# Optimization experiments

Measured on AMD Instinct MI355X. Metric: run time of the kernel, lower is better.

## Reference

```python
import jax, jax.numpy as jnp
import numpy as np

K = 4  # Chebyshev order (init kwarg k)


def _spmm(rows, cols, vals, x, n_nodes):
    # sparse [N,N] @ dense [N,D] via gather + segment_sum
    return jax.ops.segment_sum(vals[:, None] * x[cols], rows, num_segments=n_nodes)


def setup_inputs() -> dict:
    key = jax.random.key(0)
    k_x, k_r, k_c, k_v, k_w = jax.random.split(key, 5)
    N, E, D_IN, D_OUT = 50000, 800000, 128, 128
    inp = {
        "input": jax.random.normal(k_x, (N, D_IN), dtype=jnp.float32),
        "adj_rows": jax.random.randint(k_r, (E,), 0, N, dtype=jnp.int32),
        "adj_cols": jax.random.randint(k_c, (E,), 0, N, dtype=jnp.int32),
        "adj_vals": jax.random.uniform(k_v, (E,), dtype=jnp.float32) * 0.1,
        # xavier_uniform for W [in_dim, out_dim]
        "W": jax.random.uniform(k_w, (D_IN, D_OUT), dtype=jnp.float32,
                                 minval=-1.0, maxval=1.0) * np.sqrt(6.0 / (D_IN + D_OUT)),
    }
    return inp


def reference(input, adj_rows, adj_cols, adj_vals, W):
    n = input.shape[0]
    xs = []
    for i in range(K):
        if i == 0:
            xs.append(input @ W)
        elif i == 1:
            # faithful to original: support computed but unused; xs[1] == xs[0]
            xs.append(input @ W)
        else:
            support = _spmm(adj_rows, adj_cols, 2.0 * adj_vals, xs[i - 1], n) - xs[i - 2]
            xs.append(support @ W)
    return xs[-1]
```

## Files before the change

### kernel.cpp

```cpp
#include <hip/hip_runtime.h>
#include <cstddef>
#include <cstdint>

#define THREADS 256
#define KPART 256
#define MAXNB 1600

typedef short bf16x8 __attribute__((ext_vector_type(8)));
typedef float f32x4 __attribute__((ext_vector_type(4)));
typedef unsigned short u16x8 __attribute__((ext_vector_type(8)));

#define GLOBAL_AS __attribute__((address_space(1)))
#define LDS_AS    __attribute__((address_space(3)))

__device__ __forceinline__ void async_copy16(const void* g, void* l) {
    __builtin_amdgcn_global_load_lds((const GLOBAL_AS void*)g, (LDS_AS void*)l, 16, 0, 0);
}

__device__ __forceinline__ ushort f2bf(float f) {
    uint32_t u = __float_as_uint(f);
    u = u + 0x7FFFu + ((u >> 16) & 1u);
    return (ushort)(u >> 16);
}
__device__ __forceinline__ float bf2f(ushort h) {
    return __uint_as_float(((uint32_t)h) << 16);
}

__device__ __forceinline__ void rowfma(float4& acc, const float4 xv,
                                       const float4 w0, const float4 w1,
                                       const float4 w2, const float4 w3) {
    acc.x = fmaf(xv.x, w0.x, acc.x); acc.y = fmaf(xv.x, w0.y, acc.y);
    acc.z = fmaf(xv.x, w0.z, acc.z); acc.w = fmaf(xv.x, w0.w, acc.w);
    acc.x = fmaf(xv.y, w1.x, acc.x); acc.y = fmaf(xv.y, w1.y, acc.y);
    acc.z = fmaf(xv.y, w1.z, acc.z); acc.w = fmaf(xv.y, w1.w, acc.w);
    acc.x = fmaf(xv.z, w2.x, acc.x); acc.y = fmaf(xv.z, w2.y, acc.y);
    acc.z = fmaf(xv.z, w2.z, acc.z); acc.w = fmaf(xv.z, w2.w, acc.w);
    acc.x = fmaf(xv.w, w3.x, acc.x); acc.y = fmaf(xv.w, w3.y, acc.y);
    acc.z = fmaf(xv.w, w3.z, acc.z); acc.w = fmaf(xv.w, w3.w, acc.w);
}

__device__ __forceinline__ void mm32(const float4* Ws4, const float4* Xs4,
                                     int c4, int rb,
                                     float4& a0, float4& a1, float4& a2, float4& a3) {
#pragma unroll 4
    for (int kq = 0; kq < 32; ++kq) {
        float4 w0 = Ws4[(4 * kq + 0) * 32 + c4];
        float4 w1 = Ws4[(4 * kq + 1) * 32 + c4];
        float4 w2 = Ws4[(4 * kq + 2) * 32 + c4];
        float4 w3 = Ws4[(4 * kq + 3) * 32 + c4];
        float4 x0 = Xs4[(rb + 0) * 32 + kq];
        float4 x1 = Xs4[(rb + 1) * 32 + kq];
        float4 x2 = Xs4[(rb + 2) * 32 + kq];
        float4 x3 = Xs4[(rb + 3) * 32 + kq];
        rowfma(a0, x0, w0, w1, w2, w3);
        rowfma(a1, x1, w0, w1, w2, w3);
        rowfma(a2, x2, w0, w1, w2, w3);
        rowfma(a3, x3, w0, w1, w2, w3);
    }
}

__global__ __launch_bounds__(256, 2)
void wpow_kernel(const float* __restrict__ W,
                 ushort* __restrict__ w3t_hi, ushort* __restrict__ w3t_lo,
                 ushort* __restrict__ nw2t_hi, ushort* __restrict__ nw2t_lo) {
    __shared__ float4 Ws4[128 * 32];
    __shared__ float4 Xs4[32 * 32];
    const int tid = threadIdx.x;
    const int row0 = (blockIdx.x & 3) * 32;
    const bool is3 = blockIdx.x >= 4;
    const float4* __restrict__ W4 = (const float4*)W;

#pragma unroll
    for (int i = 0; i < 16; ++i) Ws4[tid + i * 256] = W4[tid + i * 256];
#pragma unroll
    for (int i = 0; i < 4; ++i) {
        int li = tid + i * 256;
        Xs4[li] = W4[(size_t)(row0 + (li >> 5)) * 32 + (li & 31)];
    }
    __syncthreads();

    const int c4 = tid & 31;
    const int rb = (tid >> 5) * 4;
    float4 a0 = {0.f, 0.f, 0.f, 0.f};
    float4 a1 = {0.f, 0.f, 0.f, 0.f};
    float4 a2 = {0.f, 0.f, 0.f, 0.f};
    float4 a3 = {0.f, 0.f, 0.f, 0.f};
    mm32(Ws4, Xs4, c4, rb, a0, a1, a2, a3);

    if (is3) {
        __syncthreads();
        Xs4[(rb + 0) * 32 + c4] = a0;
        Xs4[(rb + 1) * 32 + c4] = a1;
        Xs4[(rb + 2) * 32 + c4] = a2;
        Xs4[(rb + 3) * 32 + c4] = a3;
        __syncthreads();
        a0 = {0.f, 0.f, 0.f, 0.f};
        a1 = {0.f, 0.f, 0.f, 0.f};
        a2 = {0.f, 0.f, 0.f, 0.f};
        a3 = {0.f, 0.f, 0.f, 0.f};
        mm32(Ws4, Xs4, c4, rb, a0, a1, a2, a3);
    }

    ushort* __restrict__ dh = is3 ? w3t_hi : nw2t_hi;
    ushort* __restrict__ dl = is3 ? w3t_lo : nw2t_lo;
    const float sgn = is3 ? 1.0f : -1.0f;
    const int r = row0 + rb;
#pragma unroll
    for (int i = 0; i < 4; ++i) {
        float4 a = (i == 0) ? a0 : (i == 1) ? a1 : (i == 2) ? a2 : a3;
        const int k = r + i;
#pragma unroll
        for (int e = 0; e < 4; ++e) {
            float v = ((e == 0) ? a.x : (e == 1) ? a.y : (e == 2) ? a.z : a.w) * sgn;
            int c = c4 * 4 + e;
            int idx = c * 128 + (k ^ ((c & 7) << 3));
            ushort h = f2bf(v);
            dh[idx] = h;
            dl[idx] = f2bf(v - bf2f(h));
        }
    }
}

__global__ __launch_bounds__(256, 2)
void gemm_dual_mfma(const float* __restrict__ A1, const ushort* __restrict__ B1h,
                    const ushort* __restrict__ B1l,
                    const float* __restrict__ A2, const ushort* __restrict__ B2h,
                    const ushort* __restrict__ B2l,
                    float* __restrict__ out, int N) {
    __shared__ ushort WtHi[16384];
    __shared__ ushort WtLo[16384];
    __shared__ ushort XsHi[4096];
    __shared__ ushort XsLo[4096];
    const int tid = threadIdx.x;
    const int row0 = blockIdx.x * 32;
    const int l = tid & 63, w = tid >> 6;
    const int mt = w & 1, ntb = (w >> 1) * 4;
    const int fr = l & 15, fh = l >> 4;

    f32x4 acc[4];
#pragma unroll
    for (int nt = 0; nt < 4; ++nt) acc[nt] = (f32x4){0.f, 0.f, 0.f, 0.f};

    for (int pass = 0; pass < 2; ++pass) {
        const float* __restrict__ Asrc = pass ? A2 : A1;
        const ushort* __restrict__ Bh = pass ? B2h : B1h;
        const ushort* __restrict__ Bl = pass ? B2l : B1l;
        if (pass) __syncthreads();

#pragma unroll
        for (int i = 0; i < 8; ++i) {
            async_copy16(Bh + tid * 8 + i * 2048, WtHi + tid * 8 + i * 2048);
            async_copy16(Bl + tid * 8 + i * 2048, WtLo + tid * 8 + i * 2048);
        }

        {
            const int row = tid >> 3, kb = (tid & 7) * 16;
            int gr = row0 + row;
            if (gr >= N) gr = N - 1;
            const float4* __restrict__ ap =
                (const float4*)(Asrc + (size_t)gr * 128) + (kb >> 2);
            float4 v0 = ap[0], v1 = ap[1], v2 = ap[2], v3 = ap[3];
            float f[16] = {v0.x, v0.y, v0.z, v0.w, v1.x, v1.y, v1.z, v1.w,
                           v2.x, v2.y, v2.z, v2.w, v3.x, v3.y, v3.z, v3.w};
            ushort hi[16], lo[16];
#pragma unroll
            for (int i = 0; i < 16; ++i) {
                hi[i] = f2bf(f[i]);
                lo[i] = f2bf(f[i] - bf2f(hi[i]));
            }
#pragma unroll
            for (int g = 0; g < 2; ++g) {
                int idx = row * 128 + ((kb + 8 * g) ^ ((row & 7) << 3));
                bf16x8 vh, vl;
#pragma unroll
                for (int j = 0; j < 8; ++j) {
                    vh[j] = (short)hi[8 * g + j];
                    vl[j] = (short)lo[8 * g + j];
                }
                *(bf16x8*)&XsHi[idx] = vh;
                *(bf16x8*)&XsLo[idx] = vl;
            }
        }
        __syncthreads();

#pragma unroll
        for (int ks = 0; ks < 4; ++ks) {
            const int arow = mt * 16 + fr;
            const int aoff = arow * 128 + ((ks * 32 + fh * 8) ^ ((arow & 7) << 3));
            bf16x8 ah = *(const bf16x8*)&XsHi[aoff];
            bf16x8 al = *(const bf16x8*)&XsLo[aoff];
#pragma unroll
            for (int nt = 0; nt < 4; ++nt) {
                const int brow = (ntb + nt) * 16 + fr;
                const int boff = brow * 128 + ((ks * 32 + fh * 8) ^ ((brow & 7) << 3));
                bf16x8 bh = *(const bf16x8*)&WtHi[boff];
                bf16x8 bl = *(const bf16x8*)&WtLo[boff];
                acc[nt] = __builtin_amdgcn_mfma_f32_16x16x32_bf16(ah, bh, acc[nt], 0, 0, 0);
                acc[nt] = __builtin_amdgcn_mfma_f32_16x16x32_bf16(al, bh, acc[nt], 0, 0, 0);
                acc[nt] = __builtin_amdgcn_mfma_f32_16x16x32_bf16(ah, bl, acc[nt], 0, 0, 0);
            }
        }
    }

#pragma unroll
    for (int nt = 0; nt < 4; ++nt) {
        const int col = (ntb + nt) * 16 + fr;
#pragma unroll
        for (int i = 0; i < 4; ++i) {
            const int rr = row0 + mt * 16 + fh * 4 + i;
            if (rr < N) out[(size_t)rr * 128 + col] = acc[nt][i];
        }
    }
}

__global__ void part_count_conv_kernel(const int* __restrict__ erows, int E,
                                       int* __restrict__ blockcounts, int NB, int chunk,
                                       const float* __restrict__ X,
                                       ushort* __restrict__ Xbf, int ngroups, int cb) {
    __shared__ int hist[MAXNB];
    const int b = blockIdx.x;
    const int tid = threadIdx.x;
    if (b < cb) {
        int i = b * 256 + tid;
        if (i < ngroups) {
            const float4* __restrict__ X4 = (const float4*)X;
            float4 v0 = X4[i * 2 + 0];
            float4 v1 = X4[i * 2 + 1];
            u16x8 o;
            o[0] = f2bf(v0.x); o[1] = f2bf(v0.y); o[2] = f2bf(v0.z); o[3] = f2bf(v0.w);
            o[4] = f2bf(v1.x); o[5] = f2bf(v1.y); o[6] = f2bf(v1.z); o[7] = f2bf(v1.w);
            ((u16x8*)Xbf)[i] = o;
        }
        return;
    }
    const int k = b - cb;
    for (int i = tid; i < NB; i += 256) hist[i] = 0;
    __syncthreads();
    const int e0 = k * chunk;
    const int e1 = (e0 + chunk < E) ? e0 + chunk : E;
    for (int i = e0 + tid; i < e1; i += 256)
        atomicAdd(&hist[erows[i] >> 5], 1);
    __syncthreads();
    for (int i = tid; i < NB; i += 256) blockcounts[i * KPART + k] = hist[i];
}

__global__ void part_scan1_kernel(int* __restrict__ blockcounts,
                                  int* __restrict__ btotal, int NB) {
    const int tid = threadIdx.x;
    const int lane = tid & 63;
    const int b = blockIdx.x * 4 + (tid >> 6);
    if (b >= NB) return;
    int* __restrict__ row = blockcounts + (size_t)b * KPART;
    int c0 = row[lane * 4 + 0];
    int c1 = row[lane * 4 + 1];
    int c2 = row[lane * 4 + 2];
    int c3 = row[lane * 4 + 3];
    int lsum = c0 + c1 + c2 + c3;
    int s = lsum;
#pragma unroll
    for (int off = 1; off < 64; off <<= 1) {
        int t = __shfl_up(s, off);
        if (lane >= off) s += t;
    }
    int run = s - lsum;
    row[lane * 4 + 0] = run; run += c0;
    row[lane * 4 + 1] = run; run += c1;
    row[lane * 4 + 2] = run; run += c2;
    row[lane * 4 + 3] = run;
    if (lane == 63) btotal[b] = s;
}

__global__ __launch_bounds__(1024)
void part_scan2_kernel(const int* __restrict__ btotal, int* __restrict__ bbase,
                       int NB, int E, int* __restrict__ rowptr, int N) {
    __shared__ int sums[1024];
    const int tid = threadIdx.x;
    const int items = (NB + 1023) >> 10;
    const int start = tid * items;
    const int end = (start + items < NB) ? start + items : NB;
    int s = 0;
    for (int i = start; i < end; ++i) s += btotal[i];
    sums[tid] = s;
    __syncthreads();
#pragma unroll
    for (int off = 1; off < 1024; off <<= 1) {
        int t = (tid >= off) ? sums[tid - off] : 0;
        __syncthreads();
        sums[tid] += t;
        __syncthreads();
    }
    int run = sums[tid] - s;
    for (int i = start; i < end; ++i) {
        bbase[i] = run;
        run += btotal[i];
    }
    if (tid == 0) { bbase[NB] = E; rowptr[N] = E; }
}

__global__ void part_place_kernel(const int* __restrict__ erows,
                                  const int* __restrict__ ecols,
                                  const float* __restrict__ evals, int E,
                                  const int* __restrict__ blockcounts,
                                  const int* __restrict__ bbase, int NB, int chunk,
                                  int2* __restrict__ bucketed) {
    __shared__ int cur[MAXNB];
    const int k = blockIdx.x;
    const int tid = threadIdx.x;
    for (int i = tid; i < NB; i += 256)
        cur[i] = bbase[i] + blockcounts[(size_t)i * KPART + k];
    __syncthreads();
    const int e0 = k * chunk;
    const int e1 = (e0 + chunk < E) ? e0 + chunk : E;
    for (int i = e0 + tid; i < e1; i += 256) {
        int r = erows[i];
        int pos = atomicAdd(&cur[r >> 5], 1);
        int2 p;
        p.x = (int)(((uint32_t)(r & 31) << 16) | (uint32_t)ecols[i]);
        p.y = __float_as_int(2.0f * evals[i]);
        bucketed[pos] = p;
    }
}

__global__ void part_finish_kernel(const int2* __restrict__ bucketed,
                                   const int* __restrict__ bbase,
                                   int* __restrict__ rowptr,
                                   int2* __restrict__ csr, int N) {
    __shared__ int rcnt[32];
    __shared__ int rpos[32];
    const int b = blockIdx.x;
    const int tid = threadIdx.x;
    const int base = bbase[b];
    const int end = bbase[b + 1];
    const int row0 = b * 32;
    if (tid < 32) rcnt[tid] = 0;
    __syncthreads();
    for (int i = base + tid; i < end; i += 256)
        atomicAdd(&rcnt[((uint32_t)bucketed[i].x) >> 16], 1);
    __syncthreads();
    if (tid == 0) {
        int run = base;
        for (int j = 0; j < 32; ++j) {
            int c = rcnt[j];
            rpos[j] = run;
            if (row0 + j < N) rowptr[row0 + j] = run;
            run += c;
        }
    }
    __syncthreads();
    for (int i = base + tid; i < end; i += 256) {
        int2 e = bucketed[i];
        uint32_t meta = (uint32_t)e.x;
        int pos = atomicAdd(&rpos[meta >> 16], 1);
        int2 p;
        p.x = (int)(meta & 0xFFFFu);
        p.y = e.y;
        csr[pos] = p;
    }
}

__device__ __forceinline__ void bf8_fma(float4& aLo, float4& aHi, uint4 v, float s) {
    aLo.x = fmaf(s, __uint_as_float(v.x << 16), aLo.x);
    aLo.y = fmaf(s, __uint_as_float(v.x & 0xFFFF0000u), aLo.y);
    aLo.z = fmaf(s, __uint_as_float(v.y << 16), aLo.z);
    aLo.w = fmaf(s, __uint_as_float(v.y & 0xFFFF0000u), aLo.w);
    aHi.x = fmaf(s, __uint_as_float(v.z << 16), aHi.x);
    aHi.y = fmaf(s, __uint_as_float(v.z & 0xFFFF0000u), aHi.y);
    aHi.z = fmaf(s, __uint_as_float(v.w << 16), aHi.z);
    aHi.w = fmaf(s, __uint_as_float(v.w & 0xFFFF0000u), aHi.w);
}

template <bool WRITE_BF>
__global__ __launch_bounds__(256, 6)
void spmm_gather_bf(const int* __restrict__ rowptr, const int2* __restrict__ csr,
                    const ushort* __restrict__ src, const float* __restrict__ init,
                    void* __restrict__ dst, int N) {
    long long idx = (long long)blockIdx.x * blockDim.x + threadIdx.x;
    int row = (int)(idx >> 4);
    if (row >= N) return;
    int lane = (int)(idx & 15);
    const uint4* __restrict__ S = (const uint4*)src;
    float4 aLo0 = {0.f, 0.f, 0.f, 0.f}, aHi0 = {0.f, 0.f, 0.f, 0.f};
    float4 aLo1 = {0.f, 0.f, 0.f, 0.f}, aHi1 = {0.f, 0.f, 0.f, 0.f};
    if (init) {
        const float4* __restrict__ ip = (const float4*)init + (size_t)row * 32 + lane * 2;
        float4 t0 = ip[0], t1 = ip[1];
        aLo0.x = -t0.x; aLo0.y = -t0.y; aLo0.z = -t0.z; aLo0.w = -t0.w;
        aHi0.x = -t1.x; aHi0.y = -t1.y; aHi0.z = -t1.z; aHi0.w = -t1.w;
    }
    int p = rowptr[row];
    const int p1 = rowptr[row + 1];
    for (; p + 7 < p1; p += 8) {
        int2 cv0 = csr[p + 0];
        int2 cv1 = csr[p + 1];
        int2 cv2 = csr[p + 2];
        int2 cv3 = csr[p + 3];
        int2 cv4 = csr[p + 4];
        int2 cv5 = csr[p + 5];
        int2 cv6 = csr[p + 6];
        int2 cv7 = csr[p + 7];
        uint4 x0 = S[(size_t)cv0.x * 16 + lane];
        uint4 x1 = S[(size_t)cv1.x * 16 + lane];
        uint4 x2 = S[(size_t)cv2.x * 16 + lane];
        uint4 x3 = S[(size_t)cv3.x * 16 + lane];
        uint4 x4 = S[(size_t)cv4.x * 16 + lane];
        uint4 x5 = S[(size_t)cv5.x * 16 + lane];
        uint4 x6 = S[(size_t)cv6.x * 16 + lane];
        uint4 x7 = S[(size_t)cv7.x * 16 + lane];
        bf8_fma(aLo0, aHi0, x0, __int_as_float(cv0.y));
        bf8_fma(aLo1, aHi1, x1, __int_as_float(cv1.y));
        bf8_fma(aLo0, aHi0, x2, __int_as_float(cv2.y));
        bf8_fma(aLo1, aHi1, x3, __int_as_float(cv3.y));
        bf8_fma(aLo0, aHi0, x4, __int_as_float(cv4.y));
        bf8_fma(aLo1, aHi1, x5, __int_as_float(cv5.y));
        bf8_fma(aLo0, aHi0, x6, __int_as_float(cv6.y));
        bf8_fma(aLo1, aHi1, x7, __int_as_float(cv7.y));
    }
    for (; p + 3 < p1; p += 4) {
        int2 cv0 = csr[p + 0];
        int2 cv1 = csr[p + 1];
        int2 cv2 = csr[p + 2];
        int2 cv3 = csr[p + 3];
        uint4 x0 = S[(size_t)cv0.x * 16 + lane];
        uint4 x1 = S[(size_t)cv1.x * 16 + lane];
        uint4 x2 = S[(size_t)cv2.x * 16 + lane];
        uint4 x3 = S[(size_t)cv3.x * 16 + lane];
        bf8_fma(aLo0, aHi0, x0, __int_as_float(cv0.y));
        bf8_fma(aLo1, aHi1, x1, __int_as_float(cv1.y));
        bf8_fma(aLo0, aHi0, x2, __int_as_float(cv2.y));
        bf8_fma(aLo1, aHi1, x3, __int_as_float(cv3.y));
    }
    for (; p < p1; ++p) {
        int2 cv = csr[p];
        uint4 x = S[(size_t)cv.x * 16 + lane];
        bf8_fma(aLo0, aHi0, x, __int_as_float(cv.y));
    }
    float4 lo, hi;
    lo.x = aLo0.x + aLo1.x; lo.y = aLo0.y + aLo1.y;
    lo.z = aLo0.z + aLo1.z; lo.w = aLo0.w + aLo1.w;
    hi.x = aHi0.x + aHi1.x; hi.y = aHi0.y + aHi1.y;
    hi.z = aHi0.z + aHi1.z; hi.w = aHi0.w + aHi1.w;
    if (WRITE_BF) {
        u16x8 o;
        o[0] = f2bf(lo.x); o[1] = f2bf(lo.y); o[2] = f2bf(lo.z); o[3] = f2bf(lo.w);
        o[4] = f2bf(hi.x); o[5] = f2bf(hi.y); o[6] = f2bf(hi.z); o[7] = f2bf(hi.w);
        ((u16x8*)dst)[(size_t)row * 16 + lane] = o;
    } else {
        float4* __restrict__ op = (float4*)dst + (size_t)row * 32 + lane * 2;
        op[0] = lo;
        op[1] = hi;
    }
}

extern "C" void kernel_launch(void* const* d_in, const int* in_sizes, int n_in,
                              void* d_out, int out_size, void* d_ws, size_t ws_size,
                              hipStream_t stream) {
    const float* X     = (const float*)d_in[0];
    const int*   erows = (const int*)d_in[1];
    const int*   ecols = (const int*)d_in[2];
    const float* evals = (const float*)d_in[3];
    const float* W     = (const float*)d_in[4];
    float* out = (float*)d_out;

    const int N = in_sizes[0] / 128;
    const int E = in_sizes[1];

    ushort* t2bf    = (ushort*)d_ws;
    float*  u2      = (float*)(t2bf + (size_t)N * 128);
    int2*   bucketed= (int2*)u2;
    ushort* xbf     = (ushort*)(u2 + (size_t)N * 128);
    ushort* wtab    = xbf + (size_t)N * 128;
    ushort* w3t_hi  = wtab;
    ushort* w3t_lo  = wtab + 16384;
    ushort* nw2t_hi = wtab + 32768;
    ushort* nw2t_lo = wtab + 49152;
    int2*   csr     = (int2*)(wtab + 65536);
    int*    rowptr  = (int*)(csr + E);
    int*    blkcnt  = rowptr + (N + 1);
    const int NB    = (N + 31) >> 5;
    int*    btotal  = blkcnt + (size_t)NB * KPART;
    int*    bbase   = btotal + NB;

    const int chunk    = (E + KPART - 1) / KPART;
    const int ngroups  = N * 16;
    const int cb       = (ngroups + 255) / 256;
    const int g_blocks = (int)(((long long)N * 16 + 255) / 256);
    const int d_blocks = (N + 31) / 32;

    wpow_kernel<<<8, THREADS, 0, stream>>>(W, w3t_hi, w3t_lo, nw2t_hi, nw2t_lo);

    part_count_conv_kernel<<<cb + KPART, THREADS, 0, stream>>>(erows, E, blkcnt, NB,
                                                               chunk, X, xbf, ngroups, cb);
    part_scan1_kernel<<<(NB + 3) / 4, THREADS, 0, stream>>>(blkcnt, btotal, NB);
    part_scan2_kernel<<<1, 1024, 0, stream>>>(btotal, bbase, NB, E, rowptr, N);
    part_place_kernel<<<KPART, THREADS, 0, stream>>>(erows, ecols, evals, E, blkcnt,
                                                     bbase, NB, chunk, bucketed);
    part_finish_kernel<<<NB, THREADS, 0, stream>>>(bucketed, bbase, rowptr, csr, N);

    spmm_gather_bf<true><<<g_blocks, THREADS, 0, stream>>>(rowptr, csr, xbf, X, t2bf, N);
    spmm_gather_bf<false><<<g_blocks, THREADS, 0, stream>>>(rowptr, csr, t2bf, nullptr, u2, N);
    gemm_dual_mfma<<<d_blocks, THREADS, 0, stream>>>(u2, w3t_hi, w3t_lo,
                                                     X, nw2t_hi, nw2t_lo, out, N);
}
```

Measured before the change: 179.8 us.

## Pack CSR entries to 32 bits and slice SpMM gather across feature quarters

CSR entries now pack a 16-bit column index and a bf16 edge value into one 32-bit word, halving index traffic. The SpMM kernels are restructured so each block handles 32 rows for one quarter of the feature dimension, with 8 lanes per row gathering 8-byte chunks. It adds nontemporal loads for CSR and a nontemporal store for the fp32 output, and takes the subtracted initial term from the bf16 copy of X instead of fp32 X. This trades numerical precision (bf16 edge weights and init) and smaller per-lane gathers for less index bandwidth and possibly better cache locality. It also assumes column indices fit in 16 bits.

```diff
diff --git a/kernel.cpp b/kernel.cpp
--- a/kernel.cpp
+++ b/kernel.cpp
@@ -324,7 +324,7 @@
 __global__ void part_finish_kernel(const int2* __restrict__ bucketed,
                                    const int* __restrict__ bbase,
                                    int* __restrict__ rowptr,
-                                   int2* __restrict__ csr, int N) {
+                                   uint32_t* __restrict__ csr, int N) {
     __shared__ int rcnt[32];
     __shared__ int rpos[32];
     const int b = blockIdx.x;
@@ -351,103 +351,95 @@
         int2 e = bucketed[i];
         uint32_t meta = (uint32_t)e.x;
         int pos = atomicAdd(&rpos[meta >> 16], 1);
-        int2 p;
-        p.x = (int)(meta & 0xFFFFu);
-        p.y = e.y;
-        csr[pos] = p;
-    }
-}
-
-__device__ __forceinline__ void bf8_fma(float4& aLo, float4& aHi, uint4 v, float s) {
-    aLo.x = fmaf(s, __uint_as_float(v.x << 16), aLo.x);
-    aLo.y = fmaf(s, __uint_as_float(v.x & 0xFFFF0000u), aLo.y);
-    aLo.z = fmaf(s, __uint_as_float(v.y << 16), aLo.z);
-    aLo.w = fmaf(s, __uint_as_float(v.y & 0xFFFF0000u), aLo.w);
-    aHi.x = fmaf(s, __uint_as_float(v.z << 16), aHi.x);
-    aHi.y = fmaf(s, __uint_as_float(v.z & 0xFFFF0000u), aHi.y);
-    aHi.z = fmaf(s, __uint_as_float(v.w << 16), aHi.z);
-    aHi.w = fmaf(s, __uint_as_float(v.w & 0xFFFF0000u), aHi.w);
-}
-
-template <bool WRITE_BF>
-__global__ __launch_bounds__(256, 6)
-void spmm_gather_bf(const int* __restrict__ rowptr, const int2* __restrict__ csr,
-                    const ushort* __restrict__ src, const float* __restrict__ init,
-                    void* __restrict__ dst, int N) {
-    long long idx = (long long)blockIdx.x * blockDim.x + threadIdx.x;
-    int row = (int)(idx >> 4);
+        csr[pos] = ((meta & 0xFFFFu) << 16) | (uint32_t)f2bf(__int_as_float(e.y));
+    }
+}
+
+__device__ __forceinline__ void fma4bf(float4& a, float v, ushort4 x) {
+    a.x = fmaf(v, bf2f(x.x), a.x);
+    a.y = fmaf(v, bf2f(x.y), a.y);
+    a.z = fmaf(v, bf2f(x.z), a.z);
+    a.w = fmaf(v, bf2f(x.w), a.w);
+}
+
+template <bool WRITE_BF, bool INIT_SUB>
+__global__ __launch_bounds__(256, 8)
+void spmm_slice(const int* __restrict__ rowptr, const uint32_t* __restrict__ csr,
+                const ushort* __restrict__ src, void* __restrict__ dst, int N) {
+    const int s = blockIdx.x & 3;
+    const int g = blockIdx.x >> 2;
+    const int fl = threadIdx.x & 7;
+    const int row = g * 32 + (threadIdx.x >> 3);
     if (row >= N) return;
-    int lane = (int)(idx & 15);
-    const uint4* __restrict__ S = (const uint4*)src;
-    float4 aLo0 = {0.f, 0.f, 0.f, 0.f}, aHi0 = {0.f, 0.f, 0.f, 0.f};
-    float4 aLo1 = {0.f, 0.f, 0.f, 0.f}, aHi1 = {0.f, 0.f, 0.f, 0.f};
-    if (init) {
-        const float4* __restrict__ ip = (const float4*)init + (size_t)row * 32 + lane * 2;
-        float4 t0 = ip[0], t1 = ip[1];
-        aLo0.x = -t0.x; aLo0.y = -t0.y; aLo0.z = -t0.z; aLo0.w = -t0.w;
-        aHi0.x = -t1.x; aHi0.y = -t1.y; aHi0.z = -t1.z; aHi0.w = -t1.w;
-    }
+    const int base = s * 8 + fl;
+    const ushort4* __restrict__ S4 = (const ushort4*)src;
+
+    float4 a0 = {0.f, 0.f, 0.f, 0.f};
+    float4 a1 = {0.f, 0.f, 0.f, 0.f};
+    if (INIT_SUB) {
+        ushort4 t = S4[(size_t)row * 32 + base];
+        a0.x = -bf2f(t.x); a0.y = -bf2f(t.y); a0.z = -bf2f(t.z); a0.w = -bf2f(t.w);
+    }
+
     int p = rowptr[row];
     const int p1 = rowptr[row + 1];
     for (; p + 7 < p1; p += 8) {
-        int2 cv0 = csr[p + 0];
-        int2 cv1 = csr[p + 1];
-        int2 cv2 = csr[p + 2];
-        int2 cv3 = csr[p + 3];
-        int2 cv4 = csr[p + 4];
-        int2 cv5 = csr[p + 5];
-        int2 cv6 = csr[p + 6];
-        int2 cv7 = csr[p + 7];
-        uint4 x0 = S[(size_t)cv0.x * 16 + lane];
-        uint4 x1 = S[(size_t)cv1.x * 16 + lane];
-        uint4 x2 = S[(size_t)cv2.x * 16 + lane];
-        uint4 x3 = S[(size_t)cv3.x * 16 + lane];
-        uint4 x4 = S[(size_t)cv4.x * 16 + lane];
-        uint4 x5 = S[(size_t)cv5.x * 16 + lane];
-        uint4 x6 = S[(size_t)cv6.x * 16 + lane];
-        uint4 x7 = S[(size_t)cv7.x * 16 + lane];
-        bf8_fma(aLo0, aHi0, x0, __int_as_float(cv0.y));
-        bf8_fma(aLo1, aHi1, x1, __int_as_float(cv1.y));
-        bf8_fma(aLo0, aHi0, x2, __int_as_float(cv2.y));
-        bf8_fma(aLo1, aHi1, x3, __int_as_float(cv3.y));
-        bf8_fma(aLo0, aHi0, x4, __int_as_float(cv4.y));
-        bf8_fma(aLo1, aHi1, x5, __int_as_float(cv5.y));
-        bf8_fma(aLo0, aHi0, x6, __int_as_float(cv6.y));
-        bf8_fma(aLo1, aHi1, x7, __int_as_float(cv7.y));
+        uint32_t e0 = __builtin_nontemporal_load(csr + p + 0);
+        uint32_t e1 = __builtin_nontemporal_load(csr + p + 1);
+        uint32_t e2 = __builtin_nontemporal_load(csr + p + 2);
+        uint32_t e3 = __builtin_nontemporal_load(csr + p + 3);
+        uint32_t e4 = __builtin_nontemporal_load(csr + p + 4);
+        uint32_t e5 = __builtin_nontemporal_load(csr + p + 5);
+        uint32_t e6 = __builtin_nontemporal_load(csr + p + 6);
+        uint32_t e7 = __builtin_nontemporal_load(csr + p + 7);
+        ushort4 x0 = S4[(size_t)(e0 >> 16) * 32 + base];
+        ushort4 x1 = S4[(size_t)(e1 >> 16) * 32 + base];
+        ushort4 x2 = S4[(size_t)(e2 >> 16) * 32 + base];
+        ushort4 x3 = S4[(size_t)(e3 >> 16) * 32 + base];
+        ushort4 x4 = S4[(size_t)(e4 >> 16) * 32 + base];
+        ushort4 x5 = S4[(size_t)(e5 >> 16) * 32 + base];
+        ushort4 x6 = S4[(size_t)(e6 >> 16) * 32 + base];
+        ushort4 x7 = S4[(size_t)(e7 >> 16) * 32 + base];
+        fma4bf(a0, bf2f((ushort)(e0 & 0xFFFFu)), x0);
+        fma4bf(a1, bf2f((ushort)(e1 & 0xFFFFu)), x1);
+        fma4bf(a0, bf2f((ushort)(e2 & 0xFFFFu)), x2);
+        fma4bf(a1, bf2f((ushort)(e3 & 0xFFFFu)), x3);
+        fma4bf(a0, bf2f((ushort)(e4 & 0xFFFFu)), x4);
+        fma4bf(a1, bf2f((ushort)(e5 & 0xFFFFu)), x5);
+        fma4bf(a0, bf2f((ushort)(e6 & 0xFFFFu)), x6);
+        fma4bf(a1, bf2f((ushort)(e7 & 0xFFFFu)), x7);
     }
     for (; p + 3 < p1; p += 4) {
-        int2 cv0 = csr[p + 0];
-        int2 cv1 = csr[p + 1];
-        int2 cv2 = csr[p + 2];
-        int2 cv3 = csr[p + 3];
-        uint4 x0 = S[(size_t)cv0.x * 16 + lane];
-        uint4 x1 = S[(size_t)cv1.x * 16 + lane];
-        uint4 x2 = S[(size_t)cv2.x * 16 + lane];
-        uint4 x3 = S[(size_t)cv3.x * 16 + lane];
-        bf8_fma(aLo0, aHi0, x0, __int_as_float(cv0.y));
-        bf8_fma(aLo1, aHi1, x1, __int_as_float(cv1.y));
-        bf8_fma(aLo0, aHi0, x2, __int_as_float(cv2.y));
-        bf8_fma(aLo1, aHi1, x3, __int_as_float(cv3.y));
+        uint32_t e0 = __builtin_nontemporal_load(csr + p + 0);
+        uint32_t e1 = __builtin_nontemporal_load(csr + p + 1);
+        uint32_t e2 = __builtin_nontemporal_load(csr + p + 2);
+        uint32_t e3 = __builtin_nontemporal_load(csr + p + 3);
+        ushort4 x0 = S4[(size_t)(e0 >> 16) * 32 + base];
+        ushort4 x1 = S4[(size_t)(e1 >> 16) * 32 + base];
+        ushort4 x2 = S4[(size_t)(e2 >> 16) * 32 + base];
+        ushort4 x3 = S4[(size_t)(e3 >> 16) * 32 + base];
+        fma4bf(a0, bf2f((ushort)(e0 & 0xFFFFu)), x0);
+        fma4bf(a1, bf2f((ushort)(e1 & 0xFFFFu)), x1);
+        fma4bf(a0, bf2f((ushort)(e2 & 0xFFFFu)), x2);
+        fma4bf(a1, bf2f((ushort)(e3 & 0xFFFFu)), x3);
     }
     for (; p < p1; ++p) {
-        int2 cv = csr[p];
-        uint4 x = S[(size_t)cv.x * 16 + lane];
-        bf8_fma(aLo0, aHi0, x, __int_as_float(cv.y));
-    }
-    float4 lo, hi;
-    lo.x = aLo0.x + aLo1.x; lo.y = aLo0.y + aLo1.y;
-    lo.z = aLo0.z + aLo1.z; lo.w = aLo0.w + aLo1.w;
-    hi.x = aHi0.x + aHi1.x; hi.y = aHi0.y + aHi1.y;
-    hi.z = aHi0.z + aHi1.z; hi.w = aHi0.w + aHi1.w;
+        uint32_t e = __builtin_nontemporal_load(csr + p);
+        ushort4 x = S4[(size_t)(e >> 16) * 32 + base];
+        fma4bf(a0, bf2f((ushort)(e & 0xFFFFu)), x);
+    }
+    float4 acc;
+    acc.x = a0.x + a1.x;
+    acc.y = a0.y + a1.y;
+    acc.z = a0.z + a1.z;
+    acc.w = a0.w + a1.w;
     if (WRITE_BF) {
-        u16x8 o;
-        o[0] = f2bf(lo.x); o[1] = f2bf(lo.y); o[2] = f2bf(lo.z); o[3] = f2bf(lo.w);
-        o[4] = f2bf(hi.x); o[5] = f2bf(hi.y); o[6] = f2bf(hi.z); o[7] = f2bf(hi.w);
-        ((u16x8*)dst)[(size_t)row * 16 + lane] = o;
+        ushort4 o;
+        o.x = f2bf(acc.x); o.y = f2bf(acc.y); o.z = f2bf(acc.z); o.w = f2bf(acc.w);
+        ((ushort4*)dst)[(size_t)row * 32 + base] = o;
     } else {
-        float4* __restrict__ op = (float4*)dst + (size_t)row * 32 + lane * 2;
-        op[0] = lo;
-        op[1] = hi;
+        f32x4 v = {acc.x, acc.y, acc.z, acc.w};
+        __builtin_nontemporal_store(v, (f32x4*)dst + (size_t)row * 32 + base);
     }
 }
 
@@ -464,27 +456,27 @@
     const int N = in_sizes[0] / 128;
     const int E = in_sizes[1];
 
-    ushort* t2bf    = (ushort*)d_ws;
-    float*  u2      = (float*)(t2bf + (size_t)N * 128);
-    int2*   bucketed= (int2*)u2;
-    ushort* xbf     = (ushort*)(u2 + (size_t)N * 128);
-    ushort* wtab    = xbf + (size_t)N * 128;
-    ushort* w3t_hi  = wtab;
-    ushort* w3t_lo  = wtab + 16384;
-    ushort* nw2t_hi = wtab + 32768;
-    ushort* nw2t_lo = wtab + 49152;
-    int2*   csr     = (int2*)(wtab + 65536);
-    int*    rowptr  = (int*)(csr + E);
-    int*    blkcnt  = rowptr + (N + 1);
-    const int NB    = (N + 31) >> 5;
-    int*    btotal  = blkcnt + (size_t)NB * KPART;
-    int*    bbase   = btotal + NB;
+    ushort*   t2bf    = (ushort*)d_ws;
+    float*    u2      = (float*)(t2bf + (size_t)N * 128);
+    int2*     bucketed= (int2*)u2;
+    ushort*   xbf     = (ushort*)(u2 + (size_t)N * 128);
+    ushort*   wtab    = xbf + (size_t)N * 128;
+    ushort*   w3t_hi  = wtab;
+    ushort*   w3t_lo  = wtab + 16384;
+    ushort*   nw2t_hi = wtab + 32768;
+    ushort*   nw2t_lo = wtab + 49152;
+    uint32_t* csr     = (uint32_t*)(wtab + 65536);
+    int*      rowptr  = (int*)(csr + E);
+    int*      blkcnt  = rowptr + (N + 1);
+    const int NB      = (N + 31) >> 5;
+    int*      btotal  = blkcnt + (size_t)NB * KPART;
+    int*      bbase   = btotal + NB;
 
     const int chunk    = (E + KPART - 1) / KPART;
     const int ngroups  = N * 16;
     const int cb       = (ngroups + 255) / 256;
-    const int g_blocks = (int)(((long long)N * 16 + 255) / 256);
     const int d_blocks = (N + 31) / 32;
+    const int sl_blocks = ((N + 31) / 32) * 4;
 
     wpow_kernel<<<8, THREADS, 0, stream>>>(W, w3t_hi, w3t_lo, nw2t_hi, nw2t_lo);
 
@@ -496,8 +488,8 @@
                                                      bbase, NB, chunk, bucketed);
     part_finish_kernel<<<NB, THREADS, 0, stream>>>(bucketed, bbase, rowptr, csr, N);
 
-    spmm_gather_bf<true><<<g_blocks, THREADS, 0, stream>>>(rowptr, csr, xbf, X, t2bf, N);
-    spmm_gather_bf<false><<<g_blocks, THREADS, 0, stream>>>(rowptr, csr, t2bf, nullptr, u2, N);
+    spmm_slice<true, true><<<sl_blocks, THREADS, 0, stream>>>(rowptr, csr, xbf, t2bf, N);
+    spmm_slice<false, false><<<sl_blocks, THREADS, 0, stream>>>(rowptr, csr, t2bf, u2, N);
     gemm_dual_mfma<<<d_blocks, THREADS, 0, stream>>>(u2, w3t_hi, w3t_lo,
                                                      X, nw2t_hi, nw2t_lo, out, N);
 }
```

New measurement: 189.5 us. 5.4% more time.
